# Performance work log

Hardware: AMD Instinct MI355X
Metric: run time of the kernel (lower is better)

## Reference

```python
import jax, jax.numpy as jnp
import numpy as np

D_MODEL = 1024
N_HEADS = 16
D_HEAD = 64


def setup_inputs() -> dict:
    key = jax.random.key(0)
    ks = jax.random.split(key, 5)
    B, T = 2, 2048
    scale = 1.0 / np.sqrt(D_MODEL)
    x = jax.random.normal(ks[0], (B, T, D_MODEL), dtype=jnp.float32)
    Wq = jax.random.normal(ks[1], (N_HEADS * D_HEAD, D_MODEL), dtype=jnp.float32) * scale
    Wk = jax.random.normal(ks[2], (N_HEADS * D_HEAD, D_MODEL), dtype=jnp.float32) * scale
    Wv = jax.random.normal(ks[3], (N_HEADS * D_HEAD, D_MODEL), dtype=jnp.float32) * scale
    Wo = jax.random.normal(ks[4], (D_MODEL, N_HEADS * D_HEAD), dtype=jnp.float32) * scale
    return {"x": x, "Wq": Wq, "Wk": Wk, "Wv": Wv, "Wo": Wo}


def reference(x, Wq, Wk, Wv, Wo):
    B, T, D = x.shape
    # Linear(y = x @ W.T), then split heads: [B, H, T, d]
    def split_heads(y):
        return y.reshape(B, T, N_HEADS, D_HEAD).transpose(0, 2, 1, 3)
    q = split_heads(x @ Wq.T)
    k = split_heads(x @ Wk.T)
    v = split_heads(x @ Wv.T)
    scale = D_HEAD ** -0.5
    # Materialized [B, H, T, T] scores, as in the original module
    scores = jnp.einsum('bhtd,bhTd->bhtT', q, k) * scale
    attn = jax.nn.softmax(scores, axis=-1)
    y = jnp.einsum('bhtT,bhTd->bhtd', attn, v)
    y = y.transpose(0, 2, 1, 3).reshape(B, T, N_HEADS * D_HEAD)
    return y @ Wo.T
```

## Files before the change

### kernel.cpp

```cpp
#include <hip/hip_runtime.h>
#include <hip/hip_bf16.h>

typedef __attribute__((ext_vector_type(8))) short bf16x8;
typedef __attribute__((ext_vector_type(4))) float f32x4;
typedef unsigned short u16t;

#define DEVINL static __device__ __forceinline__

DEVINL u16t f2bf(float f) {
  union { __hip_bfloat16 h; u16t u; } cv;
  cv.h = __float2bfloat16(f);
  return cv.u;
}

DEVINL unsigned cvt_pk_bf16(float a, float b) {
  unsigned r;
  asm("v_cvt_pk_bf16_f32 %0, %1, %2" : "=v"(r) : "v"(a), "v"(b));
  return r;
}

DEVINL void async16(void* lds, const void* g) {
  __builtin_amdgcn_global_load_lds((const __attribute__((address_space(1))) void*)g,
                                   (__attribute__((address_space(3))) void*)lds,
                                   16, 0, 0);
}

__global__ __launch_bounds__(256) void convert_bf16(
    const float* __restrict__ x,  const float* __restrict__ wq,
    const float* __restrict__ wk, const float* __restrict__ wv,
    const float* __restrict__ wo,
    u16t* __restrict__ xb, u16t* __restrict__ wqb, u16t* __restrict__ wkb,
    u16t* __restrict__ wvb, u16t* __restrict__ wob) {
  const int blk = blockIdx.x;
  const float* src; u16t* dst; size_t off;
  if (blk < 4096)      { src = x;  dst = xb;  off = (size_t)blk * 1024; }
  else if (blk < 5120) { src = wq; dst = wqb; off = (size_t)(blk - 4096) * 1024; }
  else if (blk < 6144) { src = wk; dst = wkb; off = (size_t)(blk - 5120) * 1024; }
  else if (blk < 7168) { src = wv; dst = wvb; off = (size_t)(blk - 6144) * 1024; }
  else                 { src = wo; dst = wob; off = (size_t)(blk - 7168) * 1024; }
  const size_t i = off + (size_t)threadIdx.x * 4;
  const float4 v = *(const float4*)&src[i];
  ushort4 r;
  r.x = f2bf(v.x); r.y = f2bf(v.y); r.z = f2bf(v.z); r.w = f2bf(v.w);
  *(ushort4*)&dst[i] = r;
}

template <int MODE>
__global__ __launch_bounds__(256) void gemm_bt(
    const u16t* __restrict__ A, const u16t* __restrict__ B,
    void* __restrict__ C0, void* __restrict__ C1, void* __restrict__ C2,
    int M, int N, int K) {
  __shared__ u16t As[2][128 * 32];
  __shared__ u16t Bs[2][128 * 32];

  const int tid = threadIdx.x;
  const int lane = tid & 63;
  const int w = tid >> 6;
  const int wm = w >> 1, wn = w & 1;
  const int quad = lane >> 4, cl = lane & 15;
  const int m0 = blockIdx.y * 128;
  const int n0 = blockIdx.x * 128;

  const int srow = lane >> 2;
  const int scol = (lane & 3) * 8;

  f32x4 acc[4][4] = {};

  for (int k0 = 0; k0 < K; k0 += 64) {
    __syncthreads();
    #pragma unroll
    for (int p = 0; p < 2; ++p)
      #pragma unroll
      for (int ii = 0; ii < 2; ++ii) {
        const int c = w + ii * 4;
        async16(&As[p][c * 512], &A[(size_t)(m0 + c * 16 + srow) * K + k0 + p * 32 + scol]);
        async16(&Bs[p][c * 512], &B[(size_t)(n0 + c * 16 + srow) * K + k0 + p * 32 + scol]);
      }
    __syncthreads();
    #pragma unroll
    for (int p = 0; p < 2; ++p) {
      bf16x8 af[4], bfr[4];
      #pragma unroll
      for (int i = 0; i < 4; ++i)
        af[i] = *(const bf16x8*)&As[p][(wm * 64 + i * 16 + cl) * 32 + quad * 8];
      #pragma unroll
      for (int j = 0; j < 4; ++j)
        bfr[j] = *(const bf16x8*)&Bs[p][(wn * 64 + j * 16 + cl) * 32 + quad * 8];
      #pragma unroll
      for (int i = 0; i < 4; ++i)
        #pragma unroll
        for (int j = 0; j < 4; ++j)
          acc[i][j] = __builtin_amdgcn_mfma_f32_16x16x32_bf16(af[i], bfr[j], acc[i][j], 0, 0, 0);
    }
  }

  const int nz = n0 >> 10;
  #pragma unroll
  for (int i = 0; i < 4; ++i)
    #pragma unroll
    for (int j = 0; j < 4; ++j) {
      const int mb = m0 + wm * 64 + i * 16 + quad * 4;
      const int n  = n0 + wn * 64 + j * 16 + cl;
      if (MODE == 0) {
        #pragma unroll
        for (int r = 0; r < 4; ++r)
          ((float*)C0)[(size_t)(mb + r) * N + n] = acc[i][j][r];
      } else {
        const int nw = n & 1023, h = nw >> 6, d = nw & 63;
        const int b = mb >> 11, tb = mb & 2047;
        const size_t bh = (size_t)(b * 16 + h);
        if (nz == 2) {
          ushort4 v4;
          v4.x = f2bf(acc[i][j][0]); v4.y = f2bf(acc[i][j][1]);
          v4.z = f2bf(acc[i][j][2]); v4.w = f2bf(acc[i][j][3]);
          const size_t addr = (bh << 17) +
              (size_t)(((d >> 4) * 256 + (tb >> 3)) * 128 + (d & 15) * 8 + (tb & 7));
          *(ushort4*)&((u16t*)C2)[addr] = v4;
        } else if (nz == 1) {
          const size_t basea = (bh << 17) +
              (size_t)(((tb >> 4) * 8 + (d >> 3)) * 128 + (d & 7));
          #pragma unroll
          for (int r = 0; r < 4; ++r)
            ((u16t*)C1)[basea + ((tb & 15) + r) * 8] = f2bf(acc[i][j][r]);
        } else {
          #pragma unroll
          for (int r = 0; r < 4; ++r)
            ((u16t*)C0)[(bh * 2048 + tb + r) * 64 + d] =
                f2bf(acc[i][j][r] * 0.18033688011112043f);
        }
      }
    }
}

__global__ __launch_bounds__(256) void flash_attn(
    const u16t* __restrict__ Q, const u16t* __restrict__ Kt,
    const u16t* __restrict__ Vt, u16t* __restrict__ Y) {
  __shared__ u16t Ps[4 * 32 * 136];
  const int tid = threadIdx.x;
  const int lane = tid & 63;
  const int w = tid >> 6;
  const int quad = lane >> 4, cl = lane & 15;
  const int bh = blockIdx.x;
  const int q0 = blockIdx.y * 128 + w * 32;
  const u16t* Kb = Kt + ((size_t)bh << 17);
  const u16t* Vb = Vt + ((size_t)bh << 17);

  bf16x8 aq[2][2];
  #pragma unroll
  for (int h = 0; h < 2; ++h)
    #pragma unroll
    for (int ks = 0; ks < 2; ++ks)
      aq[h][ks] = *(const bf16x8*)&Q[((size_t)bh * 2048 + q0 + 16 * h + cl) * 64 + ks * 32 + quad * 8];

  bf16x8 ones8;
  #pragma unroll
  for (int i = 0; i < 8; ++i) ones8[i] = (short)0x3F80;

  f32x4 o[2][4] = {};
  f32x4 psum[2] = {};

  u16t* Pw = &Ps[w * 32 * 136];

  for (int jt = 0; jt < 16; ++jt) {
    const int j0 = jt * 128;

    f32x4 s0[8] = {}, s1[8] = {};
    #pragma unroll
    for (int ks = 0; ks < 2; ++ks) {
      bf16x8 kf[8];
      #pragma unroll
      for (int js = 0; js < 8; ++js)
        kf[js] = *(const bf16x8*)&Kb[(size_t)((((j0 >> 4) + js) * 8 + ks * 4) * 128) + lane * 8];
      #pragma unroll
      for (int js = 0; js < 8; ++js)
        s0[js] = __builtin_amdgcn_mfma_f32_16x16x32_bf16(kf[js], aq[0][ks], s0[js], 0, 0, 0);
      #pragma unroll
      for (int js = 0; js < 8; ++js)
        s1[js] = __builtin_amdgcn_mfma_f32_16x16x32_bf16(kf[js], aq[1][ks], s1[js], 0, 0, 0);
    }

    #pragma unroll
    for (int js = 0; js < 8; ++js) {
      uint2 pk0, pk1;
      pk0.x = cvt_pk_bf16(__builtin_exp2f(s0[js][0]), __builtin_exp2f(s0[js][1]));
      pk0.y = cvt_pk_bf16(__builtin_exp2f(s0[js][2]), __builtin_exp2f(s0[js][3]));
      *(uint2*)&Pw[cl * 136 + js * 16 + quad * 4] = pk0;
      pk1.x = cvt_pk_bf16(__builtin_exp2f(s1[js][0]), __builtin_exp2f(s1[js][1]));
      pk1.y = cvt_pk_bf16(__builtin_exp2f(s1[js][2]), __builtin_exp2f(s1[js][3]));
      *(uint2*)&Pw[(16 + cl) * 136 + js * 16 + quad * 4] = pk1;
    }

    #pragma unroll
    for (int ks = 0; ks < 4; ++ks) {
      const bf16x8 ap0 = *(const bf16x8*)&Pw[cl * 136 + ks * 32 + quad * 8];
      const bf16x8 ap1 = *(const bf16x8*)&Pw[(16 + cl) * 136 + ks * 32 + quad * 8];
      bf16x8 vf[4];
      #pragma unroll
      for (int ds = 0; ds < 4; ++ds)
        vf[ds] = *(const bf16x8*)&Vb[(size_t)((ds * 256 + (j0 >> 3) + ks * 4) * 128) + lane * 8];
      psum[0] = __builtin_amdgcn_mfma_f32_16x16x32_bf16(ap0, ones8, psum[0], 0, 0, 0);
      psum[1] = __builtin_amdgcn_mfma_f32_16x16x32_bf16(ap1, ones8, psum[1], 0, 0, 0);
      #pragma unroll
      for (int ds = 0; ds < 4; ++ds) {
        o[0][ds] = __builtin_amdgcn_mfma_f32_16x16x32_bf16(ap0, vf[ds], o[0][ds], 0, 0, 0);
        o[1][ds] = __builtin_amdgcn_mfma_f32_16x16x32_bf16(ap1, vf[ds], o[1][ds], 0, 0, 0);
      }
    }
  }

  const int b = bh >> 4, hd = bh & 15;
  #pragma unroll
  for (int h = 0; h < 2; ++h) {
    float inv[4];
    #pragma unroll
    for (int r = 0; r < 4; ++r) inv[r] = __builtin_amdgcn_rcpf(psum[h][r]);
    #pragma unroll
    for (int ds = 0; ds < 4; ++ds)
      #pragma unroll
      for (int r = 0; r < 4; ++r) {
        const int t = q0 + 16 * h + quad * 4 + r;
        const int d = ds * 16 + cl;
        Y[((size_t)b * 2048 + t) * 1024 + hd * 64 + d] = f2bf(o[h][ds][r] * inv[r]);
      }
  }
}

extern "C" void kernel_launch(void* const* d_in, const int* in_sizes, int n_in,
                              void* d_out, int out_size, void* d_ws, size_t ws_size,
                              hipStream_t stream) {
  (void)in_sizes; (void)n_in; (void)out_size; (void)ws_size;
  const float* x  = (const float*)d_in[0];
  const float* Wq = (const float*)d_in[1];
  const float* Wk = (const float*)d_in[2];
  const float* Wv = (const float*)d_in[3];
  const float* Wo = (const float*)d_in[4];

  char* ws = (char*)d_ws;
  const size_t MB = 1024 * 1024;
  u16t* xb  = (u16t*)(ws);
  u16t* Wqb = (u16t*)(ws + 8 * MB);
  u16t* Wkb = (u16t*)(ws + 10 * MB);
  u16t* Wvb = (u16t*)(ws + 12 * MB);
  u16t* Wob = (u16t*)(ws + 14 * MB);
  u16t* Qw  = (u16t*)(ws + 16 * MB);
  u16t* Ktw = (u16t*)(ws + 24 * MB);
  u16t* Vtw = (u16t*)(ws + 32 * MB);
  u16t* Yw  = xb;

  convert_bf16<<<8192, 256, 0, stream>>>(x, Wq, Wk, Wv, Wo, xb, Wqb, Wkb, Wvb, Wob);
  gemm_bt<1><<<dim3(24, 32), 256, 0, stream>>>(
      xb, Wqb, Qw, Ktw, Vtw, 4096, 3072, 1024);
  flash_attn<<<dim3(32, 16), 256, 0, stream>>>(Qw, Ktw, Vtw, Yw);
  gemm_bt<0><<<dim3(8, 32), 256, 0, stream>>>(
      Yw, Wob, d_out, d_out, d_out, 4096, 1024, 1024);
}
```

Before: 203.7 us.

## Double-buffer K fragments in registers and prefetch V in flash attention

Restructures the flash attention inner loop so the next tile's K fragments load into a second register buffer while the current tile is processed, with the loop unrolled by two to ping-pong the buffers. All V fragments for a tile are loaded before the P·V MFMAs, and s_setprio brackets the MFMA phases. Launch bounds now request 2 blocks per CU. The aim is to hide global load latency behind MFMA and exp work, at the cost of many more live VGPRs, which may cause spills under the occupancy constraint.

Measured after the change: 204.9 us. No clear change (+0.6%).

```diff
diff --git a/kernel.cpp b/kernel.cpp
--- a/kernel.cpp
+++ b/kernel.cpp
@@ -132,10 +132,10 @@
     }
 }
 
-__global__ __launch_bounds__(256) void flash_attn(
+__global__ __launch_bounds__(256, 2) void flash_attn(
     const u16t* __restrict__ Q, const u16t* __restrict__ Kt,
     const u16t* __restrict__ Vt, u16t* __restrict__ Y) {
-  __shared__ u16t Ps[4 * 32 * 136];
+  __shared__ u16t Ps[4][32 * 136];
   const int tid = threadIdx.x;
   const int lane = tid & 63;
   const int w = tid >> 6;
@@ -159,54 +159,78 @@
   f32x4 o[2][4] = {};
   f32x4 psum[2] = {};
 
-  u16t* Pw = &Ps[w * 32 * 136];
-
-  for (int jt = 0; jt < 16; ++jt) {
-    const int j0 = jt * 128;
-
-    f32x4 s0[8] = {}, s1[8] = {};
-    #pragma unroll
-    for (int ks = 0; ks < 2; ++ks) {
-      bf16x8 kf[8];
-      #pragma unroll
-      for (int js = 0; js < 8; ++js)
-        kf[js] = *(const bf16x8*)&Kb[(size_t)((((j0 >> 4) + js) * 8 + ks * 4) * 128) + lane * 8];
-      #pragma unroll
-      for (int js = 0; js < 8; ++js)
-        s0[js] = __builtin_amdgcn_mfma_f32_16x16x32_bf16(kf[js], aq[0][ks], s0[js], 0, 0, 0);
-      #pragma unroll
-      for (int js = 0; js < 8; ++js)
-        s1[js] = __builtin_amdgcn_mfma_f32_16x16x32_bf16(kf[js], aq[1][ks], s1[js], 0, 0, 0);
-    }
-
-    #pragma unroll
-    for (int js = 0; js < 8; ++js) {
-      uint2 pk0, pk1;
-      pk0.x = cvt_pk_bf16(__builtin_exp2f(s0[js][0]), __builtin_exp2f(s0[js][1]));
-      pk0.y = cvt_pk_bf16(__builtin_exp2f(s0[js][2]), __builtin_exp2f(s0[js][3]));
-      *(uint2*)&Pw[cl * 136 + js * 16 + quad * 4] = pk0;
-      pk1.x = cvt_pk_bf16(__builtin_exp2f(s1[js][0]), __builtin_exp2f(s1[js][1]));
-      pk1.y = cvt_pk_bf16(__builtin_exp2f(s1[js][2]), __builtin_exp2f(s1[js][3]));
-      *(uint2*)&Pw[(16 + cl) * 136 + js * 16 + quad * 4] = pk1;
-    }
-
-    #pragma unroll
-    for (int ks = 0; ks < 4; ++ks) {
-      const bf16x8 ap0 = *(const bf16x8*)&Pw[cl * 136 + ks * 32 + quad * 8];
-      const bf16x8 ap1 = *(const bf16x8*)&Pw[(16 + cl) * 136 + ks * 32 + quad * 8];
-      bf16x8 vf[4];
-      #pragma unroll
-      for (int ds = 0; ds < 4; ++ds)
-        vf[ds] = *(const bf16x8*)&Vb[(size_t)((ds * 256 + (j0 >> 3) + ks * 4) * 128) + lane * 8];
-      psum[0] = __builtin_amdgcn_mfma_f32_16x16x32_bf16(ap0, ones8, psum[0], 0, 0, 0);
-      psum[1] = __builtin_amdgcn_mfma_f32_16x16x32_bf16(ap1, ones8, psum[1], 0, 0, 0);
-      #pragma unroll
-      for (int ds = 0; ds < 4; ++ds) {
-        o[0][ds] = __builtin_amdgcn_mfma_f32_16x16x32_bf16(ap0, vf[ds], o[0][ds], 0, 0, 0);
-        o[1][ds] = __builtin_amdgcn_mfma_f32_16x16x32_bf16(ap1, vf[ds], o[1][ds], 0, 0, 0);
-      }
-    }
-  }
+  u16t* Pw = &Ps[w][0];
+
+  bf16x8 kA[2][8], kB[2][8];
+  #pragma unroll
+  for (int ks = 0; ks < 2; ++ks)
+    #pragma unroll
+    for (int js = 0; js < 8; ++js)
+      kA[ks][js] = *(const bf16x8*)&Kb[(size_t)((js * 8 + ks * 4) * 128) + lane * 8];
+
+  #define TILE_STEP(jt, kc, kn)                                               \
+  {                                                                           \
+              \
+    f32x4 s0[8] = {}, s1[8] = {};                                             \
+    __builtin_amdgcn_s_setprio(1);                                            \
+    _Pragma("unroll")                                                         \
+    for (int ks = 0; ks < 2; ++ks) {                                          \
+      _Pragma("unroll")                                                       \
+      for (int js = 0; js < 8; ++js)                                          \
+        s0[js] = __builtin_amdgcn_mfma_f32_16x16x32_bf16(kc[ks][js], aq[0][ks], s0[js], 0, 0, 0); \
+      _Pragma("unroll")                                                       \
+      for (int js = 0; js < 8; ++js)                                          \
+        s1[js] = __builtin_amdgcn_mfma_f32_16x16x32_bf16(kc[ks][js], aq[1][ks], s1[js], 0, 0, 0); \
+    }                                                                         \
+    __builtin_amdgcn_s_setprio(0);                                            \
+       \
+    _Pragma("unroll")                                                         \
+    for (int js = 0; js < 8; ++js) {                                          \
+      uint2 pk0, pk1;                                                         \
+      pk0.x = cvt_pk_bf16(__builtin_exp2f(s0[js][0]), __builtin_exp2f(s0[js][1])); \
+      pk0.y = cvt_pk_bf16(__builtin_exp2f(s0[js][2]), __builtin_exp2f(s0[js][3])); \
+      *(uint2*)&Pw[cl * 136 + js * 16 + quad * 4] = pk0;                      \
+      pk1.x = cvt_pk_bf16(__builtin_exp2f(s1[js][0]), __builtin_exp2f(s1[js][1])); \
+      pk1.y = cvt_pk_bf16(__builtin_exp2f(s1[js][2]), __builtin_exp2f(s1[js][3])); \
+      *(uint2*)&Pw[(16 + cl) * 136 + js * 16 + quad * 4] = pk1;               \
+    }                                                                         \
+                                 \
+    bf16x8 vf[4][4];                                                          \
+    _Pragma("unroll")                                                         \
+    for (int ks = 0; ks < 4; ++ks)                                            \
+      _Pragma("unroll")                                                       \
+      for (int ds = 0; ds < 4; ++ds)                                          \
+        vf[ks][ds] = *(const bf16x8*)&Vb[(size_t)((ds * 256 + (jt) * 16 + ks * 4) * 128) + lane * 8]; \
+                 \
+    if ((jt) + 1 < 16) {                                                      \
+      _Pragma("unroll")                                                       \
+      for (int ks = 0; ks < 2; ++ks)                                          \
+        _Pragma("unroll")                                                     \
+        for (int js = 0; js < 8; ++js)                                        \
+          kn[ks][js] = *(const bf16x8*)&Kb[(size_t)((((jt) + 1) * 64 + js * 8 + ks * 4) * 128) + lane * 8]; \
+    }                                                                         \
+                 \
+    __builtin_amdgcn_s_setprio(1);                                            \
+    _Pragma("unroll")                                                         \
+    for (int ks = 0; ks < 4; ++ks) {                                          \
+      const bf16x8 ap0 = *(const bf16x8*)&Pw[cl * 136 + ks * 32 + quad * 8];  \
+      const bf16x8 ap1 = *(const bf16x8*)&Pw[(16 + cl) * 136 + ks * 32 + quad * 8]; \
+      psum[0] = __builtin_amdgcn_mfma_f32_16x16x32_bf16(ap0, ones8, psum[0], 0, 0, 0); \
+      psum[1] = __builtin_amdgcn_mfma_f32_16x16x32_bf16(ap1, ones8, psum[1], 0, 0, 0); \
+      _Pragma("unroll")                                                       \
+      for (int ds = 0; ds < 4; ++ds) {                                        \
+        o[0][ds] = __builtin_amdgcn_mfma_f32_16x16x32_bf16(ap0, vf[ks][ds], o[0][ds], 0, 0, 0); \
+        o[1][ds] = __builtin_amdgcn_mfma_f32_16x16x32_bf16(ap1, vf[ks][ds], o[1][ds], 0, 0, 0); \
+      }                                                                       \
+    }                                                                         \
+    __builtin_amdgcn_s_setprio(0);                                            \
+  }
+
+  for (int jt = 0; jt < 16; jt += 2) {
+    TILE_STEP(jt, kA, kB);
+    TILE_STEP(jt + 1, kB, kA);
+  }
+  #undef TILE_STEP
 
   const int b = bh >> 4, hd = bh & 15;
   #pragma unroll
```

## Split attention KV range across two wave groups and shrink output GEMM tile

Applied to the files above, without the earlier changes.

The flash attention kernel now runs 512 threads per block, with two groups of four waves each covering half of the key/value range for the same query rows. The second group's partial outputs and row sums are reduced through shared memory before normalization, which doubles the waves in flight. This appears to rely on the softmax having no running max, so partial sums add directly. The output projection GEMM is templated on the M tile and uses BM=64, doubling its grid from 256 to 512 blocks to fill more compute units, at the cost of less B-tile reuse and more LDS per attention block.

Result: slower. 215.3 us (+5.7%).

```diff
diff --git a/kernel.cpp b/kernel.cpp
--- a/kernel.cpp
+++ b/kernel.cpp
@@ -45,12 +45,13 @@
   *(ushort4*)&dst[i] = r;
 }
 
-template <int MODE>
+template <int MODE, int BM>
 __global__ __launch_bounds__(256) void gemm_bt(
     const u16t* __restrict__ A, const u16t* __restrict__ B,
     void* __restrict__ C0, void* __restrict__ C1, void* __restrict__ C2,
     int M, int N, int K) {
-  __shared__ u16t As[2][128 * 32];
+  constexpr int MI = BM / 32;
+  __shared__ u16t As[2][BM * 32];
   __shared__ u16t Bs[2][128 * 32];
 
   const int tid = threadIdx.x;
@@ -58,36 +59,41 @@
   const int w = tid >> 6;
   const int wm = w >> 1, wn = w & 1;
   const int quad = lane >> 4, cl = lane & 15;
-  const int m0 = blockIdx.y * 128;
+  const int m0 = blockIdx.y * BM;
   const int n0 = blockIdx.x * 128;
 
   const int srow = lane >> 2;
   const int scol = (lane & 3) * 8;
 
-  f32x4 acc[4][4] = {};
+  f32x4 acc[MI][4] = {};
 
   for (int k0 = 0; k0 < K; k0 += 64) {
     __syncthreads();
     #pragma unroll
-    for (int p = 0; p < 2; ++p)
+    for (int p = 0; p < 2; ++p) {
+      #pragma unroll
+      for (int ii = 0; ii < BM / 64; ++ii) {
+        const int c = w + ii * 4;
+        async16(&As[p][c * 512], &A[(size_t)(m0 + c * 16 + srow) * K + k0 + p * 32 + scol]);
+      }
       #pragma unroll
       for (int ii = 0; ii < 2; ++ii) {
         const int c = w + ii * 4;
-        async16(&As[p][c * 512], &A[(size_t)(m0 + c * 16 + srow) * K + k0 + p * 32 + scol]);
         async16(&Bs[p][c * 512], &B[(size_t)(n0 + c * 16 + srow) * K + k0 + p * 32 + scol]);
       }
+    }
     __syncthreads();
     #pragma unroll
     for (int p = 0; p < 2; ++p) {
-      bf16x8 af[4], bfr[4];
-      #pragma unroll
-      for (int i = 0; i < 4; ++i)
-        af[i] = *(const bf16x8*)&As[p][(wm * 64 + i * 16 + cl) * 32 + quad * 8];
+      bf16x8 af[MI], bfr[4];
+      #pragma unroll
+      for (int i = 0; i < MI; ++i)
+        af[i] = *(const bf16x8*)&As[p][(wm * (BM / 2) + i * 16 + cl) * 32 + quad * 8];
       #pragma unroll
       for (int j = 0; j < 4; ++j)
         bfr[j] = *(const bf16x8*)&Bs[p][(wn * 64 + j * 16 + cl) * 32 + quad * 8];
       #pragma unroll
-      for (int i = 0; i < 4; ++i)
+      for (int i = 0; i < MI; ++i)
         #pragma unroll
         for (int j = 0; j < 4; ++j)
           acc[i][j] = __builtin_amdgcn_mfma_f32_16x16x32_bf16(af[i], bfr[j], acc[i][j], 0, 0, 0);
@@ -96,10 +102,10 @@
 
   const int nz = n0 >> 10;
   #pragma unroll
-  for (int i = 0; i < 4; ++i)
+  for (int i = 0; i < MI; ++i)
     #pragma unroll
     for (int j = 0; j < 4; ++j) {
-      const int mb = m0 + wm * 64 + i * 16 + quad * 4;
+      const int mb = m0 + wm * (BM / 2) + i * 16 + quad * 4;
       const int n  = n0 + wn * 64 + j * 16 + cl;
       if (MODE == 0) {
         #pragma unroll
@@ -132,16 +138,18 @@
     }
 }
 
-__global__ __launch_bounds__(256) void flash_attn(
+__global__ __launch_bounds__(512) void flash_attn(
     const u16t* __restrict__ Q, const u16t* __restrict__ Kt,
     const u16t* __restrict__ Vt, u16t* __restrict__ Y) {
-  __shared__ u16t Ps[4 * 32 * 136];
+  __shared__ u16t Ps[8 * 32 * 136];
   const int tid = threadIdx.x;
   const int lane = tid & 63;
   const int w = tid >> 6;
+  const int wq = w & 3;
+  const int z = w >> 2;
   const int quad = lane >> 4, cl = lane & 15;
   const int bh = blockIdx.x;
-  const int q0 = blockIdx.y * 128 + w * 32;
+  const int q0 = blockIdx.y * 128 + wq * 32;
   const u16t* Kb = Kt + ((size_t)bh << 17);
   const u16t* Vb = Vt + ((size_t)bh << 17);
 
@@ -161,7 +169,7 @@
 
   u16t* Pw = &Ps[w * 32 * 136];
 
-  for (int jt = 0; jt < 16; ++jt) {
+  for (int jt = z * 8; jt < z * 8 + 8; ++jt) {
     const int j0 = jt * 128;
 
     f32x4 s0[8] = {}, s1[8] = {};
@@ -208,20 +216,42 @@
     }
   }
 
-  const int b = bh >> 4, hd = bh & 15;
-  #pragma unroll
-  for (int h = 0; h < 2; ++h) {
-    float inv[4];
-    #pragma unroll
-    for (int r = 0; r < 4; ++r) inv[r] = __builtin_amdgcn_rcpf(psum[h][r]);
-    #pragma unroll
-    for (int ds = 0; ds < 4; ++ds)
-      #pragma unroll
-      for (int r = 0; r < 4; ++r) {
-        const int t = q0 + 16 * h + quad * 4 + r;
-        const int d = ds * 16 + cl;
-        Y[((size_t)b * 2048 + t) * 1024 + hd * 64 + d] = f2bf(o[h][ds][r] * inv[r]);
-      }
+  if (z == 1) {
+    f32x4* Po4 = (f32x4*)Pw;
+    #pragma unroll
+    for (int h = 0; h < 2; ++h)
+      #pragma unroll
+      for (int ds = 0; ds < 4; ++ds)
+        Po4[(h * 4 + ds) * 64 + lane] = o[h][ds];
+    f32x4* Pl4 = (f32x4*)((float*)Pw + 2048);
+    if (cl == 0) {
+      Pl4[quad] = psum[0];
+      Pl4[4 + quad] = psum[1];
+    }
+  }
+  __syncthreads();
+  if (z == 0) {
+    const float* Pp = (const float*)&Ps[(wq + 4) * 32 * 136];
+    const f32x4* Qo4 = (const f32x4*)Pp;
+    const f32x4* Ql4 = (const f32x4*)(Pp + 2048);
+    const int b = bh >> 4, hd = bh & 15;
+    #pragma unroll
+    for (int h = 0; h < 2; ++h) {
+      const f32x4 pt = psum[h] + Ql4[h * 4 + quad];
+      float inv[4];
+      #pragma unroll
+      for (int r = 0; r < 4; ++r) inv[r] = __builtin_amdgcn_rcpf(pt[r]);
+      #pragma unroll
+      for (int ds = 0; ds < 4; ++ds) {
+        const f32x4 ot = o[h][ds] + Qo4[(h * 4 + ds) * 64 + lane];
+        #pragma unroll
+        for (int r = 0; r < 4; ++r) {
+          const int t = q0 + 16 * h + quad * 4 + r;
+          const int d = ds * 16 + cl;
+          Y[((size_t)b * 2048 + t) * 1024 + hd * 64 + d] = f2bf(ot[r] * inv[r]);
+        }
+      }
+    }
   }
 }
 
@@ -248,9 +278,9 @@
   u16t* Yw  = xb;
 
   convert_bf16<<<8192, 256, 0, stream>>>(x, Wq, Wk, Wv, Wo, xb, Wqb, Wkb, Wvb, Wob);
-  gemm_bt<1><<<dim3(24, 32), 256, 0, stream>>>(
+  gemm_bt<1, 128><<<dim3(24, 32), 256, 0, stream>>>(
       xb, Wqb, Qw, Ktw, Vtw, 4096, 3072, 1024);
-  flash_attn<<<dim3(32, 16), 256, 0, stream>>>(Qw, Ktw, Vtw, Yw);
-  gemm_bt<0><<<dim3(8, 32), 256, 0, stream>>>(
+  flash_attn<<<dim3(32, 16), 512, 0, stream>>>(Qw, Ktw, Vtw, Yw);
+  gemm_bt<0, 64><<<dim3(8, 64), 256, 0, stream>>>(
       Yw, Wob, d_out, d_out, d_out, 4096, 1024, 1024);
 }
```
